# Optimization experiments

Hardware: AMD Instinct MI355X
Metric: run time of the kernel (lower is better)

The kernel has to match this reference:

```python
import jax, jax.numpy as jnp
import numpy as np

H = 8      # n_heads
E = 128    # d_keys (== D; required by out_projection Linear(D*n_heads, D))


def setup_inputs() -> dict:
    key = jax.random.key(0)
    ks = jax.random.split(key, 11)
    B, T, D = 64, 256, 128
    s = 0.02
    return {
        "x": jax.random.normal(ks[0], (B, T, D), dtype=jnp.float32),
        "Wq": jax.random.normal(ks[1], (D, H * E), dtype=jnp.float32) * s,
        "bq": jax.random.normal(ks[2], (H * E,), dtype=jnp.float32) * s,
        "Wk": jax.random.normal(ks[3], (D, H * E), dtype=jnp.float32) * s,
        "bk": jax.random.normal(ks[4], (H * E,), dtype=jnp.float32) * s,
        "Wv": jax.random.normal(ks[5], (D, H * E), dtype=jnp.float32) * s,
        "bv": jax.random.normal(ks[6], (H * E,), dtype=jnp.float32) * s,
        "Ws": jax.random.normal(ks[7], (T, 1), dtype=jnp.float32) * s,
        "bs": jax.random.normal(ks[8], (1,), dtype=jnp.float32) * s,
        "Wo": jax.random.normal(ks[9], (H * E, D), dtype=jnp.float32) * s,
        "bo": jax.random.normal(ks[10], (D,), dtype=jnp.float32) * s,
    }


def reference(x, Wq, bq, Wk, bk, Wv, bv, Ws, bs, Wo, bo):
    B, T, D = x.shape
    # Q/K/V projections -> [B, T, H, E]
    Q = (x @ Wq + bq).reshape(B, T, H, E)
    K = (x @ Wk + bk).reshape(B, T, H, E)
    V = (x @ Wv + bv).reshape(B, T, H, E)
    scale = 1.0 / jnp.sqrt(jnp.float32(E))
    # QK^T scores over time: [B, H, T, T] (query t, key j)
    scores = jnp.einsum('bthd,bjhd->bhtj', Q, K)
    # summary projection contracts the key axis j: T -> 1  => [B, H, T, 1]
    summary = (scale * scores) @ Ws + bs
    # softmax over the query axis t (dim=-2)
    beta = jax.nn.softmax(summary, axis=-2)[..., 0]        # [B, H, T]
    # weight V per (b, t, h) and sum over time -> [B, H, E]
    beta_cal = jnp.transpose(beta, (0, 2, 1))[..., None]   # [B, T, H, 1]
    result = jnp.sum(V * beta_cal, axis=1)                 # [B, H, E]
    out = result.reshape(B, H * E) @ Wo + bo               # [B, D]
    return out
```

## Files before the change

kernel.cpp:

```cpp
#include <hip/hip_runtime.h>
#include <hip/hip_bf16.h>


#define SCALE 0.08838834764831845f
#define MAGIC 0x13579BDFu

#define BAR() __asm__ volatile("s_waitcnt lgkmcnt(0)\n\ts_barrier" ::: "memory")

__global__ __launch_bounds__(512)
void ta_one(const float* __restrict__ x,  const float* __restrict__ Wq,
            const float* __restrict__ Wk, const float* __restrict__ bk,
            const float* __restrict__ Wv, const float* __restrict__ bv,
            const float* __restrict__ Wsv,
            const float* __restrict__ Wo, const float* __restrict__ bov,
            float* __restrict__ ws, float* __restrict__ out)
{
    __shared__ __align__(16) float pA[2056];
    __shared__ __align__(16) float pB[2056];
    __shared__ __align__(16) float wsS[256];
    __shared__ __align__(16) float xwS[128];
    __shared__ __align__(16) float kwS[256];
    __shared__ __align__(16) float wqkS[256];
    __shared__ __align__(16) float betaS[2][256];
    __shared__ __align__(16) float xbS[256];
    __shared__ __align__(16) float resS[256];
    __shared__ float smx[2][4], sms[2][4];
    __shared__ float swS;

    const int tid = threadIdx.x;
    const int b = blockIdx.x, p = blockIdx.y;
    const int w = tid >> 6, l = tid & 63;
    const float* xp0 = x + (size_t)b * 32768;

    const int q5 = tid & 31, tc = tid >> 5;
    const int q6 = tid & 63, kh = tid >> 6;
    const int c8 = tid & 7,  r8 = tid >> 3;

    float4 rx[16];
    {
        const float4* xp = (const float4*)(xp0 + (size_t)(tc * 16) * 128 + 4 * q5);
        #pragma unroll
        for (int j = 0; j < 16; ++j) rx[j] = xp[(size_t)j * 32];
    }
    float4 rwk[16];
    {
        const float4* wp = (const float4*)(Wk + (size_t)(kh * 16) * 1024 + 256 * p + 4 * q6);
        #pragma unroll
        for (int j = 0; j < 16; ++j) rwk[j] = wp[(size_t)j * 256];
    }
    const float bkv = bk[256 * p + (tid & 255)];
    const float bvv = bv[256 * p + (tid & 255)];
    if (tid < 64) *(float4*)(wsS + 4 * tid) = *(const float4*)(Wsv + 4 * tid);
    BAR();

    {
        float4 acc = {0.f, 0.f, 0.f, 0.f};
        #pragma unroll
        for (int j = 0; j < 16; ++j) {
            const float s = wsS[tc * 16 + j];
            acc.x += s * rx[j].x; acc.y += s * rx[j].y;
            acc.z += s * rx[j].z; acc.w += s * rx[j].w;
        }
        *(float4*)(pA + tc * 128 + 4 * q5) = acc;
    }
    float4 rwq[16];
    {
        #pragma unroll
        for (int rr = 0; rr < 4; ++rr) {
            const int o = r8 + 64 * rr;
            const float* base = Wq + (size_t)(o & 127) * 1024 + (2 * p + (o >> 7)) * 128;
            #pragma unroll
            for (int jj = 0; jj < 4; ++jj)
                rwq[rr * 4 + jj] = *(const float4*)(base + (jj * 8 + c8) * 4);
        }
    }
    BAR();
    if (tid < 128) {
        float v = 0.f;
        #pragma unroll
        for (int g = 0; g < 16; ++g) v += pA[g * 128 + tid];
        xwS[tid] = v;
    } else if (tid < 192) {
        float v = wsS[l] + wsS[l + 64] + wsS[l + 128] + wsS[l + 192];
        #pragma unroll
        for (int off = 32; off; off >>= 1) v += __shfl_xor(v, off, 64);
        if (l == 0) swS = v;
    }
    BAR();

    {
        float4 acc = {0.f, 0.f, 0.f, 0.f};
        #pragma unroll
        for (int j = 0; j < 16; ++j) {
            const float xv = xwS[kh * 16 + j];
            acc.x += xv * rwk[j].x; acc.y += xv * rwk[j].y;
            acc.z += xv * rwk[j].z; acc.w += xv * rwk[j].w;
        }
        *(float4*)(pB + kh * 256 + 4 * q6) = acc;
    }
    float4 rxd[16];
    {
        #pragma unroll
        for (int rr = 0; rr < 4; ++rr) {
            const int t = r8 + 64 * rr;
            const float* base = xp0 + (size_t)t * 128;
            #pragma unroll
            for (int jj = 0; jj < 4; ++jj)
                rxd[rr * 4 + jj] = *(const float4*)(base + (jj * 8 + c8) * 4);
        }
    }
    BAR();
    if (tid < 256) {
        float v = swS * bkv;
        #pragma unroll
        for (int g = 0; g < 8; ++g) v += pB[g * 256 + tid];
        kwS[tid] = v;
    }
    BAR();

    {
        #pragma unroll
        for (int rr = 0; rr < 4; ++rr) {
            const int o = r8 + 64 * rr;
            const float* kp = kwS + (o >> 7) * 128;
            float a = 0.f;
            #pragma unroll
            for (int jj = 0; jj < 4; ++jj) {
                const float4 wv = rwq[rr * 4 + jj];
                const float* kk = kp + (jj * 8 + c8) * 4;
                a += wv.x * kk[0] + wv.y * kk[1] + wv.z * kk[2] + wv.w * kk[3];
            }
            pA[c8 * 257 + o] = a;
        }
    }
    BAR();
    if (tid < 256) {
        float v = 0.f;
        #pragma unroll
        for (int g = 0; g < 8; ++g) v += pA[g * 257 + tid];
        wqkS[tid] = v * SCALE;
    }
    BAR();

    {
        #pragma unroll
        for (int rr = 0; rr < 4; ++rr) {
            const int t = r8 + 64 * rr;
            float a0 = 0.f, a1 = 0.f;
            #pragma unroll
            for (int jj = 0; jj < 4; ++jj) {
                const float4 xv = rxd[rr * 4 + jj];
                const float* q0 = wqkS + (jj * 8 + c8) * 4;
                const float* q1 = wqkS + 128 + (jj * 8 + c8) * 4;
                a0 += xv.x * q0[0] + xv.y * q0[1] + xv.z * q0[2] + xv.w * q0[3];
                a1 += xv.x * q1[0] + xv.y * q1[1] + xv.z * q1[2] + xv.w * q1[3];
            }
            pA[c8 * 257 + t] = a0;
            pB[c8 * 257 + t] = a1;
        }
    }
    float4 rxe[16];
    {
        const float4* xp = (const float4*)(xp0 + (size_t)(tc * 16) * 128 + 4 * q5);
        #pragma unroll
        for (int j = 0; j < 16; ++j) rxe[j] = xp[(size_t)j * 32];
    }
    BAR();

    {
        const int t = tid & 255, hi = tid >> 8;
        const float* pS = hi ? pB : pA;
        float v = 0.f;
        #pragma unroll
        for (int g = 0; g < 8; ++g) v += pS[g * 257 + t];
        float m = v;
        #pragma unroll
        for (int off = 32; off; off >>= 1) m = fmaxf(m, __shfl_xor(m, off, 64));
        if (l == 0) smx[hi][w & 3] = m;
        BAR();
        const float M = fmaxf(fmaxf(smx[hi][0], smx[hi][1]), fmaxf(smx[hi][2], smx[hi][3]));
        const float e = __expf(v - M);
        float ssum = e;
        #pragma unroll
        for (int off = 32; off; off >>= 1) ssum += __shfl_xor(ssum, off, 64);
        if (l == 0) sms[hi][w & 3] = ssum;
        BAR();
        const float S = sms[hi][0] + sms[hi][1] + sms[hi][2] + sms[hi][3];
        betaS[hi][t] = e / S;
    }
    BAR();

    {
        float4 a0 = {0.f,0.f,0.f,0.f}, a1 = {0.f,0.f,0.f,0.f};
        #pragma unroll
        for (int j = 0; j < 16; ++j) {
            const float b0 = betaS[0][tc * 16 + j], b1 = betaS[1][tc * 16 + j];
            a0.x += b0 * rxe[j].x; a0.y += b0 * rxe[j].y;
            a0.z += b0 * rxe[j].z; a0.w += b0 * rxe[j].w;
            a1.x += b1 * rxe[j].x; a1.y += b1 * rxe[j].y;
            a1.z += b1 * rxe[j].z; a1.w += b1 * rxe[j].w;
        }
        *(float4*)(pA + tc * 128 + 4 * q5) = a0;
        *(float4*)(pB + tc * 128 + 4 * q5) = a1;
    }
    float4 rwv[16];
    {
        const float4* wp = (const float4*)(Wv + (size_t)(kh * 16) * 1024 + 256 * p + 4 * q6);
        #pragma unroll
        for (int j = 0; j < 16; ++j) rwv[j] = wp[(size_t)j * 256];
    }
    BAR();
    if (tid < 256) {
        const int hi = tid >> 7, d = tid & 127;
        const float* pp = hi ? pB : pA;
        float v = 0.f;
        #pragma unroll
        for (int g = 0; g < 16; ++g) v += pp[g * 128 + d];
        xbS[tid] = v;
    }
    BAR();

    {
        const int hi = q6 >> 5;
        float4 acc = {0.f, 0.f, 0.f, 0.f};
        #pragma unroll
        for (int j = 0; j < 16; ++j) {
            const float xv = xbS[hi * 128 + kh * 16 + j];
            acc.x += xv * rwv[j].x; acc.y += xv * rwv[j].y;
            acc.z += xv * rwv[j].z; acc.w += xv * rwv[j].w;
        }
        *(float4*)(pB + kh * 256 + 4 * q6) = acc;
    }
    float4 rwo[16];
    {
        const float4* wp = (const float4*)(Wo + (size_t)(256 * p + tc * 16) * 128 + 4 * q5);
        #pragma unroll
        for (int j = 0; j < 16; ++j) rwo[j] = wp[(size_t)j * 32];
    }
    BAR();
    if (tid < 256) {
        float v = bvv;
        #pragma unroll
        for (int g = 0; g < 8; ++g) v += pB[g * 256 + tid];
        resS[tid] = v;
    }
    BAR();

    {
        float4 acc = {0.f, 0.f, 0.f, 0.f};
        #pragma unroll
        for (int j = 0; j < 16; ++j) {
            const float rv = resS[tc * 16 + j];
            acc.x += rv * rwo[j].x; acc.y += rv * rwo[j].y;
            acc.z += rv * rwo[j].z; acc.w += rv * rwo[j].w;
        }
        *(float4*)(pA + tc * 128 + 4 * q5) = acc;
    }
    __syncthreads();

    float* part = ws;
    unsigned* flags = (unsigned*)(ws + 32768);
    if (p < 3) {
        if (tid < 128) {
            float v = 0.f;
            #pragma unroll
            for (int g = 0; g < 16; ++g) v += pA[g * 128 + tid];
            part[(size_t)(b * 4 + p) * 128 + tid] = v;
            __threadfence();
        }
        __syncthreads();
        if (tid == 0) atomicExch(&flags[b * 4 + p], MAGIC);
    } else {
        if (tid == 0) {
            while (atomicCAS(&flags[b * 4 + 0], MAGIC, MAGIC) != MAGIC) {}
            while (atomicCAS(&flags[b * 4 + 1], MAGIC, MAGIC) != MAGIC) {}
            while (atomicCAS(&flags[b * 4 + 2], MAGIC, MAGIC) != MAGIC) {}
        }
        __syncthreads();
        if (tid < 128) {
            float v = bov[tid];
            #pragma unroll
            for (int g = 0; g < 16; ++g) v += pA[g * 128 + tid];
            v += atomicAdd(&part[(size_t)(b * 4 + 0) * 128 + tid], 0.f);
            v += atomicAdd(&part[(size_t)(b * 4 + 1) * 128 + tid], 0.f);
            v += atomicAdd(&part[(size_t)(b * 4 + 2) * 128 + tid], 0.f);
            out[(size_t)b * 128 + tid] = v;
        }
    }
}

extern "C" void kernel_launch(void* const* d_in, const int* in_sizes, int n_in,
                              void* d_out, int out_size, void* d_ws, size_t ws_size,
                              hipStream_t stream) {
    const float* x  = (const float*)d_in[0];
    const float* Wq = (const float*)d_in[1];
    const float* Wk = (const float*)d_in[3];
    const float* bk = (const float*)d_in[4];
    const float* Wv = (const float*)d_in[5];
    const float* bv = (const float*)d_in[6];
    const float* Ws = (const float*)d_in[7];
    const float* Wo = (const float*)d_in[9];
    const float* bo = (const float*)d_in[10];
    float* out = (float*)d_out;
    float* ws  = (float*)d_ws;

    ta_one<<<dim3(64, 4), dim3(512), 0, stream>>>(x, Wq, Wk, bk, Wv, bv, Ws, Wo, bo, ws, out);
}
```

Before: 94.57 us.

## Split work one head per block with 256-thread blocks and register-resident x

Changes the grid from 64x4 blocks of 512 threads (two heads each) to 64x8 blocks of 256 threads (one head each), so there are twice as many blocks and occupancy can rise to two blocks per CU. Each thread now keeps 32 rows of x in registers and reuses them for the summary, score and beta-weighted sums, instead of reloading x three times. Weight tiles are read directly inside the FMA loops rather than prefetched into registers, and the cross-block reduction now waits on seven producer blocks per batch. The risks are that x is read twice as many times overall across blocks, register pressure rises from rx[32], and the last block spin-waits on more flags.

```diff
diff --git a/kernel.cpp b/kernel.cpp
--- a/kernel.cpp
+++ b/kernel.cpp
@@ -4,10 +4,9 @@
 
 #define SCALE 0.08838834764831845f
 #define MAGIC 0x13579BDFu
-
 #define BAR() __asm__ volatile("s_waitcnt lgkmcnt(0)\n\ts_barrier" ::: "memory")
 
-__global__ __launch_bounds__(512)
+__global__ __launch_bounds__(256, 2)
 void ta_one(const float* __restrict__ x,  const float* __restrict__ Wq,
             const float* __restrict__ Wk, const float* __restrict__ bk,
             const float* __restrict__ Wv, const float* __restrict__ bv,
@@ -15,70 +14,49 @@
             const float* __restrict__ Wo, const float* __restrict__ bov,
             float* __restrict__ ws, float* __restrict__ out)
 {
-    __shared__ __align__(16) float pA[2056];
-    __shared__ __align__(16) float pB[2056];
+    __shared__ __align__(16) float buf[8224];
+    __shared__ __align__(16) float pB[1024];
     __shared__ __align__(16) float wsS[256];
     __shared__ __align__(16) float xwS[128];
-    __shared__ __align__(16) float kwS[256];
-    __shared__ __align__(16) float wqkS[256];
-    __shared__ __align__(16) float betaS[2][256];
-    __shared__ __align__(16) float xbS[256];
-    __shared__ __align__(16) float resS[256];
-    __shared__ float smx[2][4], sms[2][4];
+    __shared__ __align__(16) float kwS[128];
+    __shared__ __align__(16) float wqkS[128];
+    __shared__ __align__(16) float betaS[256];
+    __shared__ __align__(16) float xbS[128];
+    __shared__ __align__(16) float resS[128];
+    __shared__ float smx[4], sms[4];
     __shared__ float swS;
 
     const int tid = threadIdx.x;
-    const int b = blockIdx.x, p = blockIdx.y;
+    const int b = blockIdx.x, h = blockIdx.y;
     const int w = tid >> 6, l = tid & 63;
+    const int q  = tid & 31, tc = tid >> 5;
+    const int c8 = tid & 7,  r8 = tid >> 3;
     const float* xp0 = x + (size_t)b * 32768;
 
-    const int q5 = tid & 31, tc = tid >> 5;
-    const int q6 = tid & 63, kh = tid >> 6;
-    const int c8 = tid & 7,  r8 = tid >> 3;
-
-    float4 rx[16];
-    {
-        const float4* xp = (const float4*)(xp0 + (size_t)(tc * 16) * 128 + 4 * q5);
-        #pragma unroll
-        for (int j = 0; j < 16; ++j) rx[j] = xp[(size_t)j * 32];
-    }
-    float4 rwk[16];
-    {
-        const float4* wp = (const float4*)(Wk + (size_t)(kh * 16) * 1024 + 256 * p + 4 * q6);
-        #pragma unroll
-        for (int j = 0; j < 16; ++j) rwk[j] = wp[(size_t)j * 256];
-    }
-    const float bkv = bk[256 * p + (tid & 255)];
-    const float bvv = bv[256 * p + (tid & 255)];
+    float4 rx[32];
+    #pragma unroll
+    for (int j = 0; j < 32; ++j)
+        rx[j] = ((const float4*)(xp0 + (size_t)(tc * 32 + j) * 128))[q];
+    const float bkv = bk[h * 128 + (tid & 127)];
+    const float bvv = bv[h * 128 + (tid & 127)];
     if (tid < 64) *(float4*)(wsS + 4 * tid) = *(const float4*)(Wsv + 4 * tid);
     BAR();
 
     {
         float4 acc = {0.f, 0.f, 0.f, 0.f};
         #pragma unroll
-        for (int j = 0; j < 16; ++j) {
-            const float s = wsS[tc * 16 + j];
+        for (int j = 0; j < 32; ++j) {
+            const float s = wsS[tc * 32 + j];
             acc.x += s * rx[j].x; acc.y += s * rx[j].y;
             acc.z += s * rx[j].z; acc.w += s * rx[j].w;
         }
-        *(float4*)(pA + tc * 128 + 4 * q5) = acc;
-    }
-    float4 rwq[16];
-    {
-        #pragma unroll
-        for (int rr = 0; rr < 4; ++rr) {
-            const int o = r8 + 64 * rr;
-            const float* base = Wq + (size_t)(o & 127) * 1024 + (2 * p + (o >> 7)) * 128;
-            #pragma unroll
-            for (int jj = 0; jj < 4; ++jj)
-                rwq[rr * 4 + jj] = *(const float4*)(base + (jj * 8 + c8) * 4);
-        }
-    }
-    BAR();
-    if (tid < 128) {
-        float v = 0.f;
-        #pragma unroll
-        for (int g = 0; g < 16; ++g) v += pA[g * 128 + tid];
+        *(float4*)(buf + tc * 128 + 4 * q) = acc;
+    }
+    BAR();
+    if (tid < 128) {
+        float v = 0.f;
+        #pragma unroll
+        for (int g = 0; g < 8; ++g) v += buf[g * 128 + tid];
         xwS[tid] = v;
     } else if (tid < 192) {
         float v = wsS[l] + wsS[l + 64] + wsS[l + 128] + wsS[l + 192];
@@ -92,198 +70,159 @@
         float4 acc = {0.f, 0.f, 0.f, 0.f};
         #pragma unroll
         for (int j = 0; j < 16; ++j) {
-            const float xv = xwS[kh * 16 + j];
-            acc.x += xv * rwk[j].x; acc.y += xv * rwk[j].y;
-            acc.z += xv * rwk[j].z; acc.w += xv * rwk[j].w;
-        }
-        *(float4*)(pB + kh * 256 + 4 * q6) = acc;
-    }
-    float4 rxd[16];
+            const int k = tc * 16 + j;
+            const float4 wv = ((const float4*)(Wk + (size_t)k * 1024 + h * 128))[q];
+            const float xv = xwS[k];
+            acc.x += xv * wv.x; acc.y += xv * wv.y;
+            acc.z += xv * wv.z; acc.w += xv * wv.w;
+        }
+        *(float4*)(pB + tc * 128 + 4 * q) = acc;
+    }
+    BAR();
+    if (tid < 128) {
+        float v = swS * bkv;
+        #pragma unroll
+        for (int g = 0; g < 8; ++g) v += pB[g * 128 + tid];
+        kwS[tid] = v;
+    }
+    BAR();
+
     {
         #pragma unroll
         for (int rr = 0; rr < 4; ++rr) {
-            const int t = r8 + 64 * rr;
-            const float* base = xp0 + (size_t)t * 128;
-            #pragma unroll
-            for (int jj = 0; jj < 4; ++jj)
-                rxd[rr * 4 + jj] = *(const float4*)(base + (jj * 8 + c8) * 4);
-        }
-    }
-    BAR();
-    if (tid < 256) {
-        float v = swS * bkv;
-        #pragma unroll
-        for (int g = 0; g < 8; ++g) v += pB[g * 256 + tid];
-        kwS[tid] = v;
-    }
-    BAR();
-
-    {
-        #pragma unroll
-        for (int rr = 0; rr < 4; ++rr) {
-            const int o = r8 + 64 * rr;
-            const float* kp = kwS + (o >> 7) * 128;
+            const int o = 32 * rr + r8;
+            const float* base = Wq + (size_t)o * 1024 + h * 128;
             float a = 0.f;
             #pragma unroll
-            for (int jj = 0; jj < 4; ++jj) {
-                const float4 wv = rwq[rr * 4 + jj];
-                const float* kk = kp + (jj * 8 + c8) * 4;
-                a += wv.x * kk[0] + wv.y * kk[1] + wv.z * kk[2] + wv.w * kk[3];
+            for (int m = 0; m < 4; ++m) {
+                const int j4 = c8 + 8 * m;
+                const float4 wv = *(const float4*)(base + 4 * j4);
+                const float4 kv = *(const float4*)(kwS + 4 * j4);
+                a += wv.x * kv.x + wv.y * kv.y + wv.z * kv.z + wv.w * kv.w;
             }
-            pA[c8 * 257 + o] = a;
-        }
-    }
-    BAR();
-    if (tid < 256) {
-        float v = 0.f;
-        #pragma unroll
-        for (int g = 0; g < 8; ++g) v += pA[g * 257 + tid];
+            buf[c8 * 257 + o] = a;
+        }
+    }
+    BAR();
+    if (tid < 128) {
+        float v = 0.f;
+        #pragma unroll
+        for (int g = 0; g < 8; ++g) v += buf[g * 257 + tid];
         wqkS[tid] = v * SCALE;
     }
     BAR();
 
     {
-        #pragma unroll
-        for (int rr = 0; rr < 4; ++rr) {
-            const int t = r8 + 64 * rr;
-            float a0 = 0.f, a1 = 0.f;
-            #pragma unroll
-            for (int jj = 0; jj < 4; ++jj) {
-                const float4 xv = rxd[rr * 4 + jj];
-                const float* q0 = wqkS + (jj * 8 + c8) * 4;
-                const float* q1 = wqkS + 128 + (jj * 8 + c8) * 4;
-                a0 += xv.x * q0[0] + xv.y * q0[1] + xv.z * q0[2] + xv.w * q0[3];
-                a1 += xv.x * q1[0] + xv.y * q1[1] + xv.z * q1[2] + xv.w * q1[3];
-            }
-            pA[c8 * 257 + t] = a0;
-            pB[c8 * 257 + t] = a1;
-        }
-    }
-    float4 rxe[16];
-    {
-        const float4* xp = (const float4*)(xp0 + (size_t)(tc * 16) * 128 + 4 * q5);
-        #pragma unroll
-        for (int j = 0; j < 16; ++j) rxe[j] = xp[(size_t)j * 32];
-    }
-    BAR();
-
-    {
-        const int t = tid & 255, hi = tid >> 8;
-        const float* pS = hi ? pB : pA;
-        float v = 0.f;
-        #pragma unroll
-        for (int g = 0; g < 8; ++g) v += pS[g * 257 + t];
+        const float4 qv = ((const float4*)wqkS)[q];
+        #pragma unroll
+        for (int j = 0; j < 32; ++j) {
+            const float s = rx[j].x * qv.x + rx[j].y * qv.y
+                          + rx[j].z * qv.z + rx[j].w * qv.w;
+            buf[q * 257 + tc * 32 + j] = s;
+        }
+    }
+    BAR();
+
+    {
+        float v = 0.f;
+        #pragma unroll
+        for (int g = 0; g < 32; ++g) v += buf[g * 257 + tid];
         float m = v;
         #pragma unroll
         for (int off = 32; off; off >>= 1) m = fmaxf(m, __shfl_xor(m, off, 64));
-        if (l == 0) smx[hi][w & 3] = m;
+        if (l == 0) smx[w] = m;
         BAR();
-        const float M = fmaxf(fmaxf(smx[hi][0], smx[hi][1]), fmaxf(smx[hi][2], smx[hi][3]));
+        const float M = fmaxf(fmaxf(smx[0], smx[1]), fmaxf(smx[2], smx[3]));
         const float e = __expf(v - M);
         float ssum = e;
         #pragma unroll
         for (int off = 32; off; off >>= 1) ssum += __shfl_xor(ssum, off, 64);
-        if (l == 0) sms[hi][w & 3] = ssum;
+        if (l == 0) sms[w] = ssum;
         BAR();
-        const float S = sms[hi][0] + sms[hi][1] + sms[hi][2] + sms[hi][3];
-        betaS[hi][t] = e / S;
-    }
-    BAR();
-
-    {
-        float4 a0 = {0.f,0.f,0.f,0.f}, a1 = {0.f,0.f,0.f,0.f};
+        betaS[tid] = e / (sms[0] + sms[1] + sms[2] + sms[3]);
+    }
+    BAR();
+
+    {
+        float4 acc = {0.f, 0.f, 0.f, 0.f};
+        #pragma unroll
+        for (int j = 0; j < 32; ++j) {
+            const float bb = betaS[tc * 32 + j];
+            acc.x += bb * rx[j].x; acc.y += bb * rx[j].y;
+            acc.z += bb * rx[j].z; acc.w += bb * rx[j].w;
+        }
+        *(float4*)(buf + tc * 128 + 4 * q) = acc;
+    }
+    BAR();
+    if (tid < 128) {
+        float v = 0.f;
+        #pragma unroll
+        for (int g = 0; g < 8; ++g) v += buf[g * 128 + tid];
+        xbS[tid] = v;
+    }
+    BAR();
+
+    {
+        float4 acc = {0.f, 0.f, 0.f, 0.f};
         #pragma unroll
         for (int j = 0; j < 16; ++j) {
-            const float b0 = betaS[0][tc * 16 + j], b1 = betaS[1][tc * 16 + j];
-            a0.x += b0 * rxe[j].x; a0.y += b0 * rxe[j].y;
-            a0.z += b0 * rxe[j].z; a0.w += b0 * rxe[j].w;
-            a1.x += b1 * rxe[j].x; a1.y += b1 * rxe[j].y;
-            a1.z += b1 * rxe[j].z; a1.w += b1 * rxe[j].w;
-        }
-        *(float4*)(pA + tc * 128 + 4 * q5) = a0;
-        *(float4*)(pB + tc * 128 + 4 * q5) = a1;
-    }
-    float4 rwv[16];
-    {
-        const float4* wp = (const float4*)(Wv + (size_t)(kh * 16) * 1024 + 256 * p + 4 * q6);
-        #pragma unroll
-        for (int j = 0; j < 16; ++j) rwv[j] = wp[(size_t)j * 256];
-    }
-    BAR();
-    if (tid < 256) {
-        const int hi = tid >> 7, d = tid & 127;
-        const float* pp = hi ? pB : pA;
-        float v = 0.f;
-        #pragma unroll
-        for (int g = 0; g < 16; ++g) v += pp[g * 128 + d];
-        xbS[tid] = v;
-    }
-    BAR();
-
-    {
-        const int hi = q6 >> 5;
+            const int dd = tc * 16 + j;
+            const float4 wv = ((const float4*)(Wv + (size_t)dd * 1024 + h * 128))[q];
+            const float xv = xbS[dd];
+            acc.x += xv * wv.x; acc.y += xv * wv.y;
+            acc.z += xv * wv.z; acc.w += xv * wv.w;
+        }
+        *(float4*)(pB + tc * 128 + 4 * q) = acc;
+    }
+    BAR();
+    if (tid < 128) {
+        float v = bvv;
+        #pragma unroll
+        for (int g = 0; g < 8; ++g) v += pB[g * 128 + tid];
+        resS[tid] = v;
+    }
+    BAR();
+
+    {
         float4 acc = {0.f, 0.f, 0.f, 0.f};
         #pragma unroll
         for (int j = 0; j < 16; ++j) {
-            const float xv = xbS[hi * 128 + kh * 16 + j];
-            acc.x += xv * rwv[j].x; acc.y += xv * rwv[j].y;
-            acc.z += xv * rwv[j].z; acc.w += xv * rwv[j].w;
-        }
-        *(float4*)(pB + kh * 256 + 4 * q6) = acc;
-    }
-    float4 rwo[16];
-    {
-        const float4* wp = (const float4*)(Wo + (size_t)(256 * p + tc * 16) * 128 + 4 * q5);
-        #pragma unroll
-        for (int j = 0; j < 16; ++j) rwo[j] = wp[(size_t)j * 32];
-    }
-    BAR();
-    if (tid < 256) {
-        float v = bvv;
-        #pragma unroll
-        for (int g = 0; g < 8; ++g) v += pB[g * 256 + tid];
-        resS[tid] = v;
-    }
-    BAR();
-
-    {
-        float4 acc = {0.f, 0.f, 0.f, 0.f};
-        #pragma unroll
-        for (int j = 0; j < 16; ++j) {
-            const float rv = resS[tc * 16 + j];
-            acc.x += rv * rwo[j].x; acc.y += rv * rwo[j].y;
-            acc.z += rv * rwo[j].z; acc.w += rv * rwo[j].w;
-        }
-        *(float4*)(pA + tc * 128 + 4 * q5) = acc;
+            const int e = tc * 16 + j;
+            const float4 wv = ((const float4*)(Wo + (size_t)(h * 128 + e) * 128))[q];
+            const float rv = resS[e];
+            acc.x += rv * wv.x; acc.y += rv * wv.y;
+            acc.z += rv * wv.z; acc.w += rv * wv.w;
+        }
+        *(float4*)(buf + tc * 128 + 4 * q) = acc;
     }
     __syncthreads();
 
     float* part = ws;
-    unsigned* flags = (unsigned*)(ws + 32768);
-    if (p < 3) {
+    unsigned* flags = (unsigned*)(ws + 65536);
+    if (h < 7) {
         if (tid < 128) {
             float v = 0.f;
             #pragma unroll
-            for (int g = 0; g < 16; ++g) v += pA[g * 128 + tid];
-            part[(size_t)(b * 4 + p) * 128 + tid] = v;
+            for (int g = 0; g < 8; ++g) v += buf[g * 128 + tid];
+            part[(size_t)(b * 8 + h) * 128 + tid] = v;
             __threadfence();
         }
         __syncthreads();
-        if (tid == 0) atomicExch(&flags[b * 4 + p], MAGIC);
+        if (tid == 0) atomicExch(&flags[b * 8 + h], MAGIC);
     } else {
         if (tid == 0) {
-            while (atomicCAS(&flags[b * 4 + 0], MAGIC, MAGIC) != MAGIC) {}
-            while (atomicCAS(&flags[b * 4 + 1], MAGIC, MAGIC) != MAGIC) {}
-            while (atomicCAS(&flags[b * 4 + 2], MAGIC, MAGIC) != MAGIC) {}
+            #pragma unroll
+            for (int i = 0; i < 7; ++i)
+                while (atomicCAS(&flags[b * 8 + i], MAGIC, MAGIC) != MAGIC) {}
         }
         __syncthreads();
         if (tid < 128) {
             float v = bov[tid];
             #pragma unroll
-            for (int g = 0; g < 16; ++g) v += pA[g * 128 + tid];
-            v += atomicAdd(&part[(size_t)(b * 4 + 0) * 128 + tid], 0.f);
-            v += atomicAdd(&part[(size_t)(b * 4 + 1) * 128 + tid], 0.f);
-            v += atomicAdd(&part[(size_t)(b * 4 + 2) * 128 + tid], 0.f);
+            for (int g = 0; g < 8; ++g) v += buf[g * 128 + tid];
+            #pragma unroll
+            for (int i = 0; i < 7; ++i)
+                v += atomicAdd(&part[(size_t)(b * 8 + i) * 128 + tid], 0.f);
             out[(size_t)b * 128 + tid] = v;
         }
     }
@@ -304,5 +243,5 @@
     float* out = (float*)d_out;
     float* ws  = (float*)d_ws;
 
-    ta_one<<<dim3(64, 4), dim3(512), 0, stream>>>(x, Wq, Wk, bk, Wv, bv, Ws, Wo, bo, ws, out);
+    ta_one<<<dim3(64, 8), dim3(256), 0, stream>>>(x, Wq, Wk, bk, Wv, bv, Ws, Wo, bo, ws, out);
 }
```

Measured after the change: 109.8 us. +16.1%, slower.
